# Optimization experiments

Measured on AMD Instinct MI355X. Metric: run time of the kernel, lower is better.

## Reference

```python
import jax, jax.numpy as jnp
import numpy as np

HID = 768
POS = 768
TGT = 20
LBL = 30522
EPS = 1e-5


def layer_norm(x, g, b):
    mu = jnp.mean(x, axis=-1, keepdims=True)
    var = jnp.mean((x - mu) ** 2, axis=-1, keepdims=True)
    return (x - mu) * jax.lax.rsqrt(var + EPS) * g + b


def setup_inputs() -> dict:
    key = jax.random.key(0)
    ks = jax.random.split(key, 12)
    bs, n_node, num_pairs = 4, 512, 128
    inp = {
        "input_nodes": jax.random.normal(ks[0], (bs, n_node, HID), dtype=jnp.float32),
        "pairs": jax.random.randint(ks[1], (bs, num_pairs, 2), 0, n_node - 1, dtype=jnp.int64),
        "pos_emb": jax.random.normal(ks[2], (TGT, POS), dtype=jnp.float32) * 0.02,
        "W1": jax.random.normal(ks[3], (2 * HID + POS, HID), dtype=jnp.float32) * 0.02,
        "b1": jnp.zeros((HID,), dtype=jnp.float32),
        "g1": jnp.ones((HID,), dtype=jnp.float32),
        "be1": jnp.zeros((HID,), dtype=jnp.float32),
        "W2": jax.random.normal(ks[4], (HID, HID), dtype=jnp.float32) * 0.02,
        "b2": jnp.zeros((HID,), dtype=jnp.float32),
        "g2": jnp.ones((HID,), dtype=jnp.float32),
        "be2": jnp.zeros((HID,), dtype=jnp.float32),
        "Wd": jax.random.normal(ks[5], (HID, LBL), dtype=jnp.float32) * 0.02,
        "bd": jnp.zeros((LBL,), dtype=jnp.float32),
    }
    return inp


def reference(input_nodes, pairs, pos_emb, W1, b1, g1, be1, W2, b2, g2, be2, Wd, bd):
    bs, num_pairs, _ = pairs.shape
    dim = input_nodes.shape[-1]
    left = pairs[:, :, 0] + 1   # [bs, np]
    right = pairs[:, :, 1] + 1
    # gather paired node features: [bs, np, dim]
    lh = jnp.take_along_axis(input_nodes, left[:, :, None], axis=1)
    rh = jnp.take_along_axis(input_nodes, right[:, :, None], axis=1)
    R = bs * num_pairs
    lh = jnp.broadcast_to(lh.reshape(R, 1, dim), (R, TGT, dim))
    rh = jnp.broadcast_to(rh.reshape(R, 1, dim), (R, TGT, dim))
    pe = jnp.broadcast_to(pos_emb[None, :, :], (R, TGT, POS))
    x = jnp.concatenate((lh, rh, pe), axis=-1)  # [R, TGT, 2*HID+POS]
    h = layer_norm(jax.nn.gelu(x @ W1 + b1), g1, be1)
    h = layer_norm(jax.nn.gelu(h @ W2 + b2), g2, be2)
    return h @ Wd + bd  # [R, TGT, LBL]
```

## Files before the change

kernel.cpp:

```cpp
#include <hip/hip_runtime.h>
#include <stdint.h>
#include <math.h>

typedef unsigned short u16;
typedef unsigned int u32;

#define HID   768
#define TGT   20
#define LBL   30522
#define RPAIR 512
#define ROWS  10240
#define KCAT  1536
#define NPAD  30592

typedef float  f32x4  __attribute__((ext_vector_type(4)));
typedef __bf16 bf16x8 __attribute__((ext_vector_type(8)));

__device__ __forceinline__ u16 f2bf(float f) {
  u32 u = __float_as_uint(f);
  u += 0x7fffu + ((u >> 16) & 1u);
  return (u16)(u >> 16);
}
__device__ __forceinline__ float bf2f(u16 h) {
  return __uint_as_float(((u32)h) << 16);
}
__device__ __forceinline__ float gelu_tanh(float x) {
  float x3 = x * x * x;
  float t = tanhf(0.7978845608028654f * (x + 0.044715f * x3));
  return 0.5f * x * (1.0f + t);
}

__device__ __forceinline__ void async16(u16* lds, const u16* g) {
  __builtin_amdgcn_global_load_lds(
      (__attribute__((address_space(1))) void*)const_cast<u16*>(g),
      (__attribute__((address_space(3))) void*)lds,
      16, 0, 0);
}

__global__ __launch_bounds__(256) void tconv_kernel(const float* __restrict__ B,
                                                    u16* __restrict__ Bt,
                                                    int K, int N, int Npad) {
  __shared__ u16 tile[32][34];
  int n0 = blockIdx.x * 32, k0 = blockIdx.y * 32;
  int tx = threadIdx.x & 31, ty = threadIdx.x >> 5;
#pragma unroll
  for (int i = 0; i < 4; i++) {
    int kk = ty + i * 8;
    int k = k0 + kk, n = n0 + tx;
    float v = (k < K && n < N) ? B[(size_t)k * N + n] : 0.0f;
    tile[kk][tx] = f2bf(v);
  }
  __syncthreads();
#pragma unroll
  for (int i = 0; i < 4; i++) {
    int nn = ty + i * 8;
    int n = n0 + nn, k = k0 + tx;
    if (n < Npad && k < K) Bt[(size_t)n * K + k] = tile[tx][nn];
  }
}

__global__ __launch_bounds__(256) void gather_kernel(const float* __restrict__ nodes,
                                                     const int* __restrict__ p32,
                                                     u16* __restrict__ A1) {
  int idx = blockIdx.x * 256 + threadIdx.x;
  if (idx >= RPAIR * KCAT) return;
  bool is64 = ((p32[1] | p32[3] | p32[5] | p32[7] | p32[9] | p32[11] | p32[13] | p32[15]) == 0);
  int r = idx / KCAT, c = idx - r * KCAT;
  int b = r >> 7, p = r & 127;
  int which = (c >= HID) ? 1 : 0;
  int cc = which ? (c - HID) : c;
  int slot = (b * 128 + p) * 2 + which;
  int node = (is64 ? p32[slot * 2] : p32[slot]) + 1;
  float v = nodes[((size_t)(b * 512 + node)) * HID + cc];
  A1[idx] = f2bf(v);
}

__global__ __launch_bounds__(256) void peproj_kernel(const float* __restrict__ pos_emb,
                                                     const float* __restrict__ W1,
                                                     const float* __restrict__ b1,
                                                     float* __restrict__ pep) {
  __shared__ float pe[HID];
  int t = blockIdx.x, tid = threadIdx.x;
  for (int i = tid; i < HID; i += 256) pe[i] = pos_emb[t * HID + i];
  __syncthreads();
  float acc0 = 0.f, acc1 = 0.f, acc2 = 0.f;
  const float* Wp = W1 + (size_t)KCAT * HID;
  for (int k = 0; k < HID; k++) {
    float p = pe[k];
    const float* wr = Wp + (size_t)k * HID;
    acc0 = fmaf(p, wr[tid], acc0);
    acc1 = fmaf(p, wr[tid + 256], acc1);
    acc2 = fmaf(p, wr[tid + 512], acc2);
  }
  pep[t * HID + tid]       = acc0 + b1[tid];
  pep[t * HID + tid + 256] = acc1 + b1[tid + 256];
  pep[t * HID + tid + 512] = acc2 + b1[tid + 512];
}

template <int EPI>
__global__ __launch_bounds__(256) void gemm_bt(const u16* __restrict__ A,
                                               const u16* __restrict__ Bt,
                                               const float* __restrict__ bias,
                                               float* __restrict__ Cf,
                                               u16* __restrict__ Cb,
                                               int N, int K) {
  __shared__ __align__(16) u16 As[128 * 32];
  __shared__ __align__(16) u16 Bs[128 * 32];
  const int tid  = threadIdx.x;
  const int lane = tid & 63;
  const int w    = tid >> 6;
  const int wr   = w >> 1, wc = w & 1;
  const int m0 = blockIdx.y * 128;
  const int n0 = blockIdx.x * 128;

  f32x4 acc[4][4];
  const f32x4 fzero = {0.f, 0.f, 0.f, 0.f};
#pragma unroll
  for (int m = 0; m < 4; m++)
#pragma unroll
    for (int n = 0; n < 4; n++) acc[m][n] = fzero;

  const int srow = lane >> 2;
  const int scol = (lane & 3) * 8;
  const int nkt = K >> 5;

  for (int kt = 0; kt < nkt; ++kt) {
    const int k0 = kt << 5;
#pragma unroll
    for (int j = 0; j < 2; j++) {
      int rbase = w * 32 + j * 16;
      async16(&As[rbase * 32], A + (size_t)(m0 + rbase + srow) * K + k0 + scol);
      async16(&Bs[rbase * 32], Bt + (size_t)(n0 + rbase + srow) * K + k0 + scol);
    }
    asm volatile("s_waitcnt vmcnt(0)" ::: "memory");
    __syncthreads();

    bf16x8 a[4], b[4];
    const int kk = (lane >> 4) * 8;
#pragma unroll
    for (int m = 0; m < 4; m++)
      a[m] = *reinterpret_cast<const bf16x8*>(&As[(wr * 64 + m * 16 + (lane & 15)) * 32 + kk]);
#pragma unroll
    for (int n = 0; n < 4; n++)
      b[n] = *reinterpret_cast<const bf16x8*>(&Bs[(wc * 64 + n * 16 + (lane & 15)) * 32 + kk]);
#pragma unroll
    for (int m = 0; m < 4; m++)
#pragma unroll
      for (int n = 0; n < 4; n++)
        acc[m][n] = __builtin_amdgcn_mfma_f32_16x16x32_bf16(a[m], b[n], acc[m][n], 0, 0, 0);
    __syncthreads();
  }

  const int rr = (lane >> 4) * 4;
  const int cc = lane & 15;
#pragma unroll
  for (int m = 0; m < 4; m++) {
#pragma unroll
    for (int n = 0; n < 4; n++) {
      int col = n0 + wc * 64 + n * 16 + cc;
#pragma unroll
      for (int j = 0; j < 4; j++) {
        int row = m0 + wr * 64 + m * 16 + rr + j;
        float v = acc[m][n][j];
        if (EPI == 0) {
          Cf[(size_t)row * N + col] = v;
        } else {
          v = gelu_tanh(v + bias[col]);
          Cb[(size_t)row * N + col] = f2bf(v);
        }
      }
    }
  }
}

__global__ __launch_bounds__(256) void gemm128_head(const u16* __restrict__ A,
                                                    const u16* __restrict__ B,
                                                    const float* __restrict__ bias,
                                                    float* __restrict__ C) {
  __shared__ __align__(16) u16 As[2][128 * 64];
  __shared__ __align__(16) u16 Bs[2][128 * 64];
  const int tid  = threadIdx.x;
  const int lane = tid & 63;
  const int w    = tid >> 6;
  const int wr   = w >> 1, wc = w & 1;

  const int bid   = blockIdx.x;
  const int xcd   = bid & 7;
  const int idx   = bid >> 3;
  const int ntile = idx / 10;
  const int mtile = xcd * 10 + (idx - ntile * 10);
  const int m0 = mtile * 128;
  const int n0 = ntile * 128;

  f32x4 acc[4][4];
  const f32x4 fzero = {0.f, 0.f, 0.f, 0.f};
#pragma unroll
  for (int m = 0; m < 4; m++)
#pragma unroll
    for (int n = 0; n < 4; n++) acc[m][n] = fzero;

  const int sl_r = lane >> 3;
  const int sl_c = ((lane & 7) ^ sl_r) * 8;
  auto stage = [&](int buf, int kt) {
    const int k0 = kt * 64;
#pragma unroll
    for (int j = 0; j < 4; j++) {
      int rbase = w * 32 + j * 8;
      async16(&As[buf][rbase * 64], A + (size_t)(m0 + rbase + sl_r) * 768 + k0 + sl_c);
      async16(&Bs[buf][rbase * 64], B + (size_t)(n0 + rbase + sl_r) * 768 + k0 + sl_c);
    }
  };
  auto lda = [&](const u16* buf, int m, int ks) -> bf16x8 {
    int row = wr * 64 + m * 16 + (lane & 15);
    int kch = ks * 4 + (lane >> 4);
    return *reinterpret_cast<const bf16x8*>(&buf[row * 64 + ((kch ^ (row & 7)) << 3)]);
  };
  auto ldb = [&](const u16* buf, int n, int ks) -> bf16x8 {
    int row = wc * 64 + n * 16 + (lane & 15);
    int kch = ks * 4 + (lane >> 4);
    return *reinterpret_cast<const bf16x8*>(&buf[row * 64 + ((kch ^ (row & 7)) << 3)]);
  };

  const int nkt = 12;
  stage(0, 0);
  __syncthreads();

  for (int t = 0; t < nkt; ++t) {
    const int cur = t & 1;
    if (t + 1 < nkt) stage(cur ^ 1, t + 1);
    const u16* Ab = As[cur];
    const u16* Bb = Bs[cur];
#pragma unroll
    for (int ks = 0; ks < 2; ++ks) {
      bf16x8 a[4], b[4];
#pragma unroll
      for (int m = 0; m < 4; m++) a[m] = lda(Ab, m, ks);
#pragma unroll
      for (int n = 0; n < 4; n++) b[n] = ldb(Bb, n, ks);
#pragma unroll
      for (int m = 0; m < 4; m++)
#pragma unroll
        for (int n = 0; n < 4; n++)
          acc[m][n] = __builtin_amdgcn_mfma_f32_16x16x32_bf16(a[m], b[n], acc[m][n], 0, 0, 0);
    }
    __syncthreads();
  }

  const int rr = (lane >> 4) * 4;
  const int cc = lane & 15;
#pragma unroll
  for (int n = 0; n < 4; n++) {
    int col = n0 + wc * 64 + n * 16 + cc;
    if (col < LBL) {
      float bv = bias[col];
#pragma unroll
      for (int m = 0; m < 4; m++)
#pragma unroll
        for (int j = 0; j < 4; j++) {
          int row = m0 + wr * 64 + m * 16 + rr + j;
          C[(size_t)row * LBL + col] = acc[m][n][j] + bv;
        }
    }
  }
}

__global__ __launch_bounds__(256) void fuse1_kernel(const float* __restrict__ s,
                                                    const float* __restrict__ pep,
                                                    const float* __restrict__ g1,
                                                    const float* __restrict__ be1,
                                                    u16* __restrict__ h1) {
  __shared__ float red[8];
  int g = blockIdx.x, tid = threadIdx.x;
  int r = g / TGT, t = g - r * TGT;
  const float* sr = s + (size_t)r * HID;
  const float* pt = pep + (size_t)t * HID;
  float y[3], s1 = 0.f, s2 = 0.f;
#pragma unroll
  for (int i = 0; i < 3; i++) {
    int j = tid + i * 256;
    float x = sr[j] + pt[j];
    y[i] = gelu_tanh(x);
    s1 += y[i];
    s2 += y[i] * y[i];
  }
#pragma unroll
  for (int off = 32; off > 0; off >>= 1) {
    s1 += __shfl_down(s1, off);
    s2 += __shfl_down(s2, off);
  }
  if ((tid & 63) == 0) { red[tid >> 6] = s1; red[4 + (tid >> 6)] = s2; }
  __syncthreads();
  float mean = (red[0] + red[1] + red[2] + red[3]) * (1.0f / HID);
  float var  = (red[4] + red[5] + red[6] + red[7]) * (1.0f / HID) - mean * mean;
  float inv  = rsqrtf(var + 1e-5f);
#pragma unroll
  for (int i = 0; i < 3; i++) {
    int j = tid + i * 256;
    h1[(size_t)g * HID + j] = f2bf((y[i] - mean) * inv * g1[j] + be1[j]);
  }
}

__global__ __launch_bounds__(256) void fuse2_kernel(const u16* __restrict__ G,
                                                    const float* __restrict__ g2,
                                                    const float* __restrict__ be2,
                                                    u16* __restrict__ h2) {
  __shared__ float red[8];
  int g = blockIdx.x, tid = threadIdx.x;
  const u16* gr = G + (size_t)g * HID;
  float y[3], s1 = 0.f, s2 = 0.f;
#pragma unroll
  for (int i = 0; i < 3; i++) {
    int j = tid + i * 256;
    y[i] = bf2f(gr[j]);
    s1 += y[i];
    s2 += y[i] * y[i];
  }
#pragma unroll
  for (int off = 32; off > 0; off >>= 1) {
    s1 += __shfl_down(s1, off);
    s2 += __shfl_down(s2, off);
  }
  if ((tid & 63) == 0) { red[tid >> 6] = s1; red[4 + (tid >> 6)] = s2; }
  __syncthreads();
  float mean = (red[0] + red[1] + red[2] + red[3]) * (1.0f / HID);
  float var  = (red[4] + red[5] + red[6] + red[7]) * (1.0f / HID) - mean * mean;
  float inv  = rsqrtf(var + 1e-5f);
#pragma unroll
  for (int i = 0; i < 3; i++) {
    int j = tid + i * 256;
    h2[(size_t)g * HID + j] = f2bf((y[i] - mean) * inv * g2[j] + be2[j]);
  }
}

extern "C" void kernel_launch(void* const* d_in, const int* in_sizes, int n_in,
                              void* d_out, int out_size, void* d_ws, size_t ws_size,
                              hipStream_t stream) {
  const float* input_nodes = (const float*)d_in[0];
  const int*   pairs       = (const int*)d_in[1];
  const float* pos_emb     = (const float*)d_in[2];
  const float* W1  = (const float*)d_in[3];
  const float* b1  = (const float*)d_in[4];
  const float* g1  = (const float*)d_in[5];
  const float* be1 = (const float*)d_in[6];
  const float* W2  = (const float*)d_in[7];
  const float* b2  = (const float*)d_in[8];
  const float* g2  = (const float*)d_in[9];
  const float* be2 = (const float*)d_in[10];
  const float* Wd  = (const float*)d_in[11];
  const float* bd  = (const float*)d_in[12];
  float* out = (float*)d_out;

  char* ws = (char*)d_ws;
  u16*   WdT   = (u16*)(ws + 0);
  u16*   W2T   = (u16*)(ws + 46989312);
  u16*   W1lrT = (u16*)(ws + 48168960);
  u16*   A1    = (u16*)(ws + 50528256);
  float* pep   = (float*)(ws + 52101120);
  float* sbuf  = (float*)(ws + 52162560);
  u16*   h1    = (u16*)(ws + 53735424);
  u16*   G     = (u16*)(ws + 69464064);

  tconv_kernel<<<dim3(956, 24), 256, 0, stream>>>(Wd, WdT, HID, LBL, NPAD);
  tconv_kernel<<<dim3(24, 24), 256, 0, stream>>>(W2, W2T, HID, HID, HID);
  tconv_kernel<<<dim3(24, 48), 256, 0, stream>>>(W1, W1lrT, KCAT, HID, HID);
  gather_kernel<<<dim3((RPAIR * KCAT + 255) / 256), 256, 0, stream>>>(input_nodes, pairs, A1);
  peproj_kernel<<<dim3(TGT), 256, 0, stream>>>(pos_emb, W1, b1, pep);

  gemm_bt<0><<<dim3(6, 4), 256, 0, stream>>>(A1, W1lrT, nullptr, sbuf, nullptr, HID, KCAT);
  fuse1_kernel<<<dim3(ROWS), 256, 0, stream>>>(sbuf, pep, g1, be1, h1);

  gemm_bt<1><<<dim3(6, 80), 256, 0, stream>>>(h1, W2T, b2, nullptr, G, HID, HID);
  fuse2_kernel<<<dim3(ROWS), 256, 0, stream>>>(G, g2, be2, G);

  gemm128_head<<<dim3(19120), 256, 0, stream>>>(G, WdT, bd, out);
}
```

Baseline: 1.287 ms.

## Single-buffer head GEMM LDS to raise occupancy and simplify tile order

The head GEMM drops LDS double buffering in favour of a single 32KB buffer with a load-wait-sync-compute loop. It sets launch bounds to allow 5 blocks per CU and replaces the XCD-aware tile swizzle with a plain M-major block mapping. The aim is to hide memory latency through more resident blocks rather than in-block prefetch. The cost is that loads no longer overlap with MFMA inside a block, and the swizzle's L2 locality may be lost.

After: 1.442 ms. +12.1%, slower.

```diff
diff --git a/kernel.cpp b/kernel.cpp
--- a/kernel.cpp
+++ b/kernel.cpp
@@ -173,24 +173,22 @@
   }
 }
 
-__global__ __launch_bounds__(256) void gemm128_head(const u16* __restrict__ A,
+__global__ __launch_bounds__(256, 5) void gemm128v2(const u16* __restrict__ A,
                                                     const u16* __restrict__ B,
                                                     const float* __restrict__ bias,
                                                     float* __restrict__ C) {
-  __shared__ __align__(16) u16 As[2][128 * 64];
-  __shared__ __align__(16) u16 Bs[2][128 * 64];
+  __shared__ __align__(16) u16 As[128 * 64];
+  __shared__ __align__(16) u16 Bs[128 * 64];
   const int tid  = threadIdx.x;
   const int lane = tid & 63;
   const int w    = tid >> 6;
   const int wr   = w >> 1, wc = w & 1;
 
-  const int bid   = blockIdx.x;
-  const int xcd   = bid & 7;
-  const int idx   = bid >> 3;
-  const int ntile = idx / 10;
-  const int mtile = xcd * 10 + (idx - ntile * 10);
-  const int m0 = mtile * 128;
-  const int n0 = ntile * 128;
+  const int bid = blockIdx.x;
+  const int nt  = bid / 80;
+  const int mt  = bid - nt * 80;
+  const int m0  = mt * 128;
+  const int n0  = nt * 128;
 
   f32x4 acc[4][4];
   const f32x4 fzero = {0.f, 0.f, 0.f, 0.f};
@@ -201,42 +199,35 @@
 
   const int sl_r = lane >> 3;
   const int sl_c = ((lane & 7) ^ sl_r) * 8;
-  auto stage = [&](int buf, int kt) {
-    const int k0 = kt * 64;
-#pragma unroll
-    for (int j = 0; j < 4; j++) {
-      int rbase = w * 32 + j * 8;
-      async16(&As[buf][rbase * 64], A + (size_t)(m0 + rbase + sl_r) * 768 + k0 + sl_c);
-      async16(&Bs[buf][rbase * 64], B + (size_t)(n0 + rbase + sl_r) * 768 + k0 + sl_c);
-    }
-  };
-  auto lda = [&](const u16* buf, int m, int ks) -> bf16x8 {
+  auto lda = [&](int m, int ks) -> bf16x8 {
     int row = wr * 64 + m * 16 + (lane & 15);
     int kch = ks * 4 + (lane >> 4);
-    return *reinterpret_cast<const bf16x8*>(&buf[row * 64 + ((kch ^ (row & 7)) << 3)]);
+    return *reinterpret_cast<const bf16x8*>(&As[row * 64 + ((kch ^ (row & 7)) << 3)]);
   };
-  auto ldb = [&](const u16* buf, int n, int ks) -> bf16x8 {
+  auto ldb = [&](int n, int ks) -> bf16x8 {
     int row = wc * 64 + n * 16 + (lane & 15);
     int kch = ks * 4 + (lane >> 4);
-    return *reinterpret_cast<const bf16x8*>(&buf[row * 64 + ((kch ^ (row & 7)) << 3)]);
+    return *reinterpret_cast<const bf16x8*>(&Bs[row * 64 + ((kch ^ (row & 7)) << 3)]);
   };
 
-  const int nkt = 12;
-  stage(0, 0);
-  __syncthreads();
-
-  for (int t = 0; t < nkt; ++t) {
-    const int cur = t & 1;
-    if (t + 1 < nkt) stage(cur ^ 1, t + 1);
-    const u16* Ab = As[cur];
-    const u16* Bb = Bs[cur];
+  for (int kt = 0; kt < 12; ++kt) {
+    const int k0 = kt * 64;
+#pragma unroll
+    for (int jj = 0; jj < 4; jj++) {
+      int rbase = w * 32 + jj * 8;
+      async16(&As[rbase * 64], A + (size_t)(m0 + rbase + sl_r) * 768 + k0 + sl_c);
+      async16(&Bs[rbase * 64], B + (size_t)(n0 + rbase + sl_r) * 768 + k0 + sl_c);
+    }
+    asm volatile("s_waitcnt vmcnt(0)" ::: "memory");
+    __syncthreads();
+
 #pragma unroll
     for (int ks = 0; ks < 2; ++ks) {
       bf16x8 a[4], b[4];
 #pragma unroll
-      for (int m = 0; m < 4; m++) a[m] = lda(Ab, m, ks);
-#pragma unroll
-      for (int n = 0; n < 4; n++) b[n] = ldb(Bb, n, ks);
+      for (int m = 0; m < 4; m++) a[m] = lda(m, ks);
+#pragma unroll
+      for (int n = 0; n < 4; n++) b[n] = ldb(n, ks);
 #pragma unroll
       for (int m = 0; m < 4; m++)
 #pragma unroll
@@ -372,5 +363,5 @@
   gemm_bt<1><<<dim3(6, 80), 256, 0, stream>>>(h1, W2T, b2, nullptr, G, HID, HID);
   fuse2_kernel<<<dim3(ROWS), 256, 0, stream>>>(G, g2, be2, G);
 
-  gemm128_head<<<dim3(19120), 256, 0, stream>>>(G, WdT, bd, out);
-}
+  gemm128v2<<<dim3(19120), 256, 0, stream>>>(G, WdT, bd, out);
+}
```
